# Kernel optimization log

Hardware: AMD Instinct MI355X
Metric: run time of the kernel (lower is better)

The kernel has to match this reference:

```python
import jax, jax.numpy as jnp
import numpy as np

IN_CH, OUT_CH = 64, 32
V1, V2 = 40962, 163842  # icosahedral levels; V2 = 4*V1 - 6
B = 4
EPS = 1e-5
SLOPE = 0.2  # LeakyReLU negative slope


def setup_inputs() -> dict:
    key = jax.random.key(0)
    ks = jax.random.split(key, 8)
    return {
        "x1": jax.random.normal(ks[0], (B, IN_CH, V1), jnp.float32),
        "x2": jax.random.normal(ks[1], (B, OUT_CH, V2), jnp.float32),
        "neigh_orders": jax.random.randint(ks[2], (7 * V2,), 0, V2, jnp.int32),
        "upconv_top_index": jax.random.randint(ks[3], (V1,), 0, V1 * 7, jnp.int32),
        "upconv_down_index": jax.random.randint(ks[4], (2 * (V2 - V1),), 0, V1 * 7, jnp.int32),
        "W_up": jax.random.normal(ks[5], (7 * OUT_CH, IN_CH), jnp.float32) * 0.05,
        "b_up": jnp.zeros((7 * OUT_CH,), jnp.float32),
        "W1": jax.random.normal(ks[6], (OUT_CH, 7 * 2 * OUT_CH), jnp.float32) * 0.05,
        "b1": jnp.zeros((OUT_CH,), jnp.float32),
        "g1": jnp.ones((OUT_CH,), jnp.float32),
        "be1": jnp.zeros((OUT_CH,), jnp.float32),
        "W2": jax.random.normal(ks[7], (OUT_CH, 7 * OUT_CH), jnp.float32) * 0.05,
        "b2": jnp.zeros((OUT_CH,), jnp.float32),
        "g2": jnp.ones((OUT_CH,), jnp.float32),
        "be2": jnp.zeros((OUT_CH,), jnp.float32),
    }


def _bn_lrelu(x, g, b):
    # BatchNorm1d with track_running_stats=False: always uses current (per-sample) batch stats,
    # biased variance, over the vertex axis. Then LeakyReLU(0.2).
    mu = x.mean(axis=0)
    var = x.var(axis=0)  # biased (ddof=0), matches torch BN normalization
    y = (x - mu) * jax.lax.rsqrt(var + EPS) * g + b
    return jnp.where(y >= 0, y, SLOPE * y)


def _one_sample(x1b, x2b, neigh, top, down,
                W_up, b_up, W1, b1, g1, be1, W2, b2, g2, be2):
    # upconv: Linear(in_ch -> 7*out_ch), scatter to the finer mesh via index gathers
    raw = x1b.T @ W_up.T + b_up                      # (V1, 7*OUT_CH)
    flat = raw.reshape(V1 * 7, OUT_CH)
    y_top = flat[top]                                # (V1, OUT_CH)
    y_down = flat[down].reshape(-1, OUT_CH, 2).mean(axis=-1)  # (V2-V1, OUT_CH), torch view semantics
    y1 = jnp.concatenate([y_top, y_down], axis=0)    # (V2, OUT_CH)
    y = jnp.concatenate([y1, x2b.T], axis=1)         # (V2, 2*OUT_CH) skip-concat
    # one-ring conv 1: gather 7 neighbors, flatten, GEMM
    m = y[neigh].reshape(V2, 7 * 2 * OUT_CH)
    h = _bn_lrelu(m @ W1.T + b1, g1, be1)            # (V2, OUT_CH)
    # one-ring conv 2
    m2 = h[neigh].reshape(V2, 7 * OUT_CH)
    h2 = _bn_lrelu(m2 @ W2.T + b2, g2, be2)          # (V2, OUT_CH)
    return h2.T                                      # (OUT_CH, V2)


def reference(x1, x2, neigh_orders, upconv_top_index, upconv_down_index,
              W_up, b_up, W1, b1, g1, be1, W2, b2, g2, be2):
    f = lambda a, b: _one_sample(a, b, neigh_orders, upconv_top_index, upconv_down_index,
                                 W_up, b_up, W1, b1, g1, be1, W2, b2, g2, be2)
    return jax.vmap(f)(x1, x2)  # (B, OUT_CH, V2)
```

## Files before the change

### kernel.cpp

```cpp
#include <hip/hip_runtime.h>

#define V1n 40962
#define V2n 163842
#define Bn  4

typedef _Float16 h8   __attribute__((ext_vector_type(8)));
typedef float    f32x4 __attribute__((ext_vector_type(4)));

__device__ __forceinline__ float h2f(_Float16 h) { return (float)h; }

__global__ __launch_bounds__(256) void k_pack_up(const float* __restrict__ Wup,
                                                 _Float16* __restrict__ WupP) {
  int i = blockIdx.x * 256 + threadIdx.x;
  if (i >= 14336) return;
  int e = i & 7, col = (i >> 3) & 15, g = i >> 7;
  int nt = g % 14, kq = g / 14;
  int j = nt * 16 + col;
  int k = (kq >> 2) * 32 + (kq & 3) * 8 + e;
  WupP[i] = (_Float16)Wup[j * 64 + k];
}

__global__ __launch_bounds__(256, 4) void k_upconv(const float* __restrict__ x1,
    const float* __restrict__ bup, const _Float16* __restrict__ WupP,
    _Float16* __restrict__ rawq) {
  int b = blockIdx.y;
  int lane = threadIdx.x & 63, wv = threadIdx.x >> 6;
  int col = lane & 15, quad = lane >> 4;
  int v0 = blockIdx.x * 64 + wv * 16;
  int v = v0 + col;
  int vc = min(v, V1n - 1);
  const float* xb = x1 + (size_t)b * 64 * V1n + vc;
  float t0[8], t1v[8];
#pragma unroll
  for (int e = 0; e < 8; ++e) t0[e] = xb[(size_t)(quad * 8 + e) * V1n];
#pragma unroll
  for (int e = 0; e < 8; ++e) t1v[e] = xb[(size_t)(32 + quad * 8 + e) * V1n];
  h8 a0, a1;
#pragma unroll
  for (int e = 0; e < 8; ++e) { a0[e] = (_Float16)t0[e]; a1[e] = (_Float16)t1v[e]; }

  f32x4 acc[14];
#pragma unroll
  for (int nt = 0; nt < 14; ++nt) {
    float bv = bup[nt * 16 + col];
    acc[nt] = (f32x4){bv, bv, bv, bv};
  }
  const _Float16* wp0 = WupP + (size_t)(quad * 14) * 128 + col * 8;
  const _Float16* wp1 = WupP + (size_t)((4 + quad) * 14) * 128 + col * 8;
#pragma unroll
  for (int nt = 0; nt < 14; ++nt) {
    h8 b0 = *(const h8*)(wp0 + nt * 128);
    acc[nt] = __builtin_amdgcn_mfma_f32_16x16x32_f16(a0, b0, acc[nt], 0, 0, 0);
  }
#pragma unroll
  for (int nt = 0; nt < 14; ++nt) {
    h8 b1 = *(const h8*)(wp1 + nt * 128);
    acc[nt] = __builtin_amdgcn_mfma_f32_16x16x32_f16(a1, b1, acc[nt], 0, 0, 0);
  }
  __shared__ _Float16 tile[4][3584];
  _Float16* tw = tile[wv];
#pragma unroll
  for (int nt = 0; nt < 14; ++nt)
#pragma unroll
    for (int r = 0; r < 4; ++r)
      tw[(quad * 4 + r) * 224 + nt * 16 + col] = (_Float16)acc[nt][r];
  __syncthreads();
  _Float16* dst = rawq + ((size_t)b * V1n + v0) * 224;
  int rem = V1n - v0;
  if (rem >= 16) {
#pragma unroll
    for (int i = 0; i < 7; ++i)
      *(h8*)(dst + i * 512 + lane * 8) = *(const h8*)(tw + i * 512 + lane * 8);
  } else if (rem > 0) {
    for (int i = 0; i < 7; ++i) {
      int off = i * 512 + lane * 8;
      if (off / 224 < rem) *(h8*)(dst + off) = *(const h8*)(tw + off);
    }
  }
}

__global__ __launch_bounds__(256) void k_assemble(const float* __restrict__ x2,
    const int* __restrict__ top, const int* __restrict__ down,
    const _Float16* __restrict__ rawq, _Float16* __restrict__ y) {
  int b = blockIdx.y;
  int v = blockIdx.x * 256 + threadIdx.x;
  if (v >= V2n) return;
  const _Float16* rb = rawq + (size_t)b * V1n * 224;
  h8 r0, r1, r2, r3;
  if (v < V1n) {
    int f = top[v];
    const _Float16* src = rb + (size_t)(f / 7) * 224 + (f % 7) * 32;
    r0 = *(const h8*)src;        r1 = *(const h8*)(src + 8);
    r2 = *(const h8*)(src + 16); r3 = *(const h8*)(src + 24);
  } else {
    int k = v - V1n;
    int d0 = down[2 * k], d1 = down[2 * k + 1];
    const _Float16* se = rb + (size_t)(d0 / 7) * 224 + (d0 % 7) * 32;
    const _Float16* so = rb + (size_t)(d1 / 7) * 224 + (d1 % 7) * 32;
    h8 a0 = *(const h8*)se,        a1 = *(const h8*)(se + 8);
    h8 a2 = *(const h8*)(se + 16), a3 = *(const h8*)(se + 24);
    h8 c0 = *(const h8*)so,        c1 = *(const h8*)(so + 8);
    h8 c2 = *(const h8*)(so + 16), c3 = *(const h8*)(so + 24);
#pragma unroll
    for (int i = 0; i < 4; ++i) {
      r0[i]     = (_Float16)(0.5f * (h2f(a0[2 * i]) + h2f(a0[2 * i + 1])));
      r0[4 + i] = (_Float16)(0.5f * (h2f(a1[2 * i]) + h2f(a1[2 * i + 1])));
      r1[i]     = (_Float16)(0.5f * (h2f(a2[2 * i]) + h2f(a2[2 * i + 1])));
      r1[4 + i] = (_Float16)(0.5f * (h2f(a3[2 * i]) + h2f(a3[2 * i + 1])));
      r2[i]     = (_Float16)(0.5f * (h2f(c0[2 * i]) + h2f(c0[2 * i + 1])));
      r2[4 + i] = (_Float16)(0.5f * (h2f(c1[2 * i]) + h2f(c1[2 * i + 1])));
      r3[i]     = (_Float16)(0.5f * (h2f(c2[2 * i]) + h2f(c2[2 * i + 1])));
      r3[4 + i] = (_Float16)(0.5f * (h2f(c3[2 * i]) + h2f(c3[2 * i + 1])));
    }
  }
  _Float16* dst = y + ((size_t)b * V2n + v) * 64;
  *(h8*)(dst)      = r0; *(h8*)(dst + 8)  = r1;
  *(h8*)(dst + 16) = r2; *(h8*)(dst + 24) = r3;
  const float* xp = x2 + (size_t)b * 32 * V2n + v;
#pragma unroll
  for (int g2 = 0; g2 < 4; ++g2) {
    h8 px;
#pragma unroll
    for (int e = 0; e < 8; ++e) px[e] = (_Float16)xp[(size_t)(g2 * 8 + e) * V2n];
    *(h8*)(dst + 32 + g2 * 8) = px;
  }
}

__global__ __launch_bounds__(256) void k_pack(const float* __restrict__ W1,
    const float* __restrict__ W2, _Float16* __restrict__ W1p,
    _Float16* __restrict__ W2p) {
  int i = blockIdx.x * 256 + threadIdx.x;
  if (i < 14336) {
    int e = i & 7, o = (i >> 3) & 31, g = i >> 8;
    int k = (g >> 2) * 32 + (g & 3) * 8 + e;
    W1p[i] = (_Float16)W1[o * 448 + k];
  }
  int i2 = i - 14336;
  if (i2 >= 0 && i2 < 7168) {
    int e = i2 & 7, o = (i2 >> 3) & 31, g = i2 >> 8;
    int k = (g >> 2) * 32 + (g & 3) * 8 + e;
    W2p[i2] = (_Float16)W2[o * 224 + k];
  }
}

__global__ __launch_bounds__(256, 4) void k_conv1(const _Float16* __restrict__ y,
    const int* __restrict__ neigh, const _Float16* __restrict__ W1p,
    _Float16* __restrict__ t1, float* __restrict__ sumsR) {
  int b = blockIdx.y;
  int lane = threadIdx.x & 63, wv = threadIdx.x >> 6;
  int col = lane & 15, quad = lane >> 4;
  int v0 = blockIdx.x * 64 + wv * 16;
  int v = v0 + col;
  int vc = min(v, V2n - 1);
  const int* np = neigh + 7 * (size_t)vc;
  int idx[7];
#pragma unroll
  for (int j = 0; j < 7; ++j) idx[j] = np[j];
  const _Float16* yb = y + (size_t)b * V2n * 64 + quad * 8;
  h8 a[14];
#pragma unroll
  for (int j = 0; j < 7; ++j) {
    const _Float16* r = yb + (size_t)idx[j] * 64;
    a[2 * j]     = *(const h8*)r;
    a[2 * j + 1] = *(const h8*)(r + 32);
  }
  f32x4 acc0 = {0.f, 0.f, 0.f, 0.f}, acc1 = {0.f, 0.f, 0.f, 0.f};
  const _Float16* wp = W1p + quad * 256;
#pragma unroll
  for (int kt = 0; kt < 14; ++kt) {
    h8 b0 = *(const h8*)(wp + (size_t)kt * 1024 + col * 8);
    h8 b1 = *(const h8*)(wp + (size_t)kt * 1024 + (16 + col) * 8);
    acc0 = __builtin_amdgcn_mfma_f32_16x16x32_f16(a[kt], b0, acc0, 0, 0, 0);
    acc1 = __builtin_amdgcn_mfma_f32_16x16x32_f16(a[kt], b1, acc1, 0, 0, 0);
  }
  __shared__ _Float16 tile[4][16][32];
  __shared__ float red[4][4][16];
#pragma unroll
  for (int r = 0; r < 4; ++r) {
    tile[wv][quad * 4 + r][col]      = (_Float16)acc0[r];
    tile[wv][quad * 4 + r][16 + col] = (_Float16)acc1[r];
  }
  __syncthreads();
  int row = threadIdx.x >> 2, ch = threadIdx.x & 3;
  int vv = blockIdx.x * 64 + row;
  float s[8], q[8];
#pragma unroll
  for (int e = 0; e < 8; ++e) { s[e] = 0.f; q[e] = 0.f; }
  if (vv < V2n) {
    h8 val = *(const h8*)&tile[row >> 4][row & 15][ch * 8];
    *(h8*)(t1 + ((size_t)b * V2n + vv) * 32 + ch * 8) = val;
#pragma unroll
    for (int e = 0; e < 8; ++e) { float x = h2f(val[e]); s[e] = x; q[e] = x * x; }
  }
#pragma unroll
  for (int m = 4; m <= 32; m <<= 1) {
#pragma unroll
    for (int e = 0; e < 8; ++e) { s[e] += __shfl_xor(s[e], m); q[e] += __shfl_xor(q[e], m); }
  }
  if (lane < 4) {
#pragma unroll
    for (int e = 0; e < 8; ++e) { red[wv][lane][e] = s[e]; red[wv][lane][8 + e] = q[e]; }
  }
  __syncthreads();
  if (threadIdx.x < 64) {
    int chh = threadIdx.x >> 4, e = threadIdx.x & 15;
    float v4 = red[0][chh][e] + red[1][chh][e] + red[2][chh][e] + red[3][chh][e];
    int c = chh * 8 + (e & 7);
    int rep = blockIdx.x & 63;
    float* dst = sumsR + rep * 256 + ((e < 8) ? (b * 32 + c) : (128 + b * 32 + c));
    atomicAdd(dst, v4);
  }
}

__global__ void k_finalize(const float* __restrict__ sumsR, const float* __restrict__ g,
                           const float* __restrict__ be, float* __restrict__ sc,
                           float* __restrict__ sh) {
  int i = threadIdx.x;
  if (i >= 128) return;
  float s = 0.f, q = 0.f;
  for (int r = 0; r < 64; ++r) { s += sumsR[r * 256 + i]; q += sumsR[r * 256 + 128 + i]; }
  float inv = 1.0f / (float)V2n;
  float mu = s * inv;
  float var = fmaf(q, inv, -mu * mu);
  float rs = rsqrtf(var + 1e-5f);
  int o = i & 31;
  float scale = rs * g[o];
  sc[i] = scale;
  sh[i] = fmaf(-mu, scale, be[o]);
}

__global__ __launch_bounds__(256, 4) void k_conv2(const _Float16* __restrict__ t1,
    const int* __restrict__ neigh, const _Float16* __restrict__ W2p,
    const float* __restrict__ sc1, const float* __restrict__ sh1,
    float* __restrict__ out, float* __restrict__ sumsR) {
  int b = blockIdx.y;
  int lane = threadIdx.x & 63, wv = threadIdx.x >> 6;
  int col = lane & 15, quad = lane >> 4;
  int v0 = blockIdx.x * 64 + wv * 16;
  int v = v0 + col;
  int vc = min(v, V2n - 1);
  const int* np = neigh + 7 * (size_t)vc;
  int idx[7];
#pragma unroll
  for (int j = 0; j < 7; ++j) idx[j] = np[j];
  const _Float16* tb = t1 + (size_t)b * V2n * 32 + quad * 8;
  h8 raw[7];
#pragma unroll
  for (int j = 0; j < 7; ++j) raw[j] = *(const h8*)(tb + (size_t)idx[j] * 32);
  float sc[8], sh[8];
#pragma unroll
  for (int i = 0; i < 8; ++i) {
    sc[i] = sc1[b * 32 + quad * 8 + i];
    sh[i] = sh1[b * 32 + quad * 8 + i];
  }
  f32x4 acc0 = {0.f, 0.f, 0.f, 0.f}, acc1 = {0.f, 0.f, 0.f, 0.f};
  const _Float16* wp = W2p + quad * 256;
#pragma unroll
  for (int j = 0; j < 7; ++j) {
    h8 a;
#pragma unroll
    for (int e = 0; e < 8; ++e) {
      float f = fmaf(h2f(raw[j][e]), sc[e], sh[e]);
      f = fmaxf(f, 0.2f * f);
      a[e] = (_Float16)f;
    }
    h8 b0 = *(const h8*)(wp + (size_t)j * 1024 + col * 8);
    h8 b1 = *(const h8*)(wp + (size_t)j * 1024 + (16 + col) * 8);
    acc0 = __builtin_amdgcn_mfma_f32_16x16x32_f16(a, b0, acc0, 0, 0, 0);
    acc1 = __builtin_amdgcn_mfma_f32_16x16x32_f16(a, b1, acc1, 0, 0, 0);
  }
  float* ob = out + (size_t)b * 32 * V2n;
  int vrow = v0 + quad * 4;
  float s0 = 0.f, q0 = 0.f, s1 = 0.f, q1 = 0.f;
  if (blockIdx.x != gridDim.x - 1) {
    float* p0 = ob + (size_t)col * V2n + vrow;
    *(float2*)p0       = make_float2(acc0[0], acc0[1]);
    *(float2*)(p0 + 2) = make_float2(acc0[2], acc0[3]);
    float* p1 = ob + (size_t)(16 + col) * V2n + vrow;
    *(float2*)p1       = make_float2(acc1[0], acc1[1]);
    *(float2*)(p1 + 2) = make_float2(acc1[2], acc1[3]);
#pragma unroll
    for (int r = 0; r < 4; ++r) {
      s0 += acc0[r]; q0 += acc0[r] * acc0[r];
      s1 += acc1[r]; q1 += acc1[r] * acc1[r];
    }
  } else {
#pragma unroll
    for (int r = 0; r < 4; ++r) {
      if (vrow + r < V2n) {
        ob[(size_t)col * V2n + vrow + r]        = acc0[r];
        ob[(size_t)(16 + col) * V2n + vrow + r] = acc1[r];
        s0 += acc0[r]; q0 += acc0[r] * acc0[r];
        s1 += acc1[r]; q1 += acc1[r] * acc1[r];
      }
    }
  }
#pragma unroll
  for (int m = 16; m <= 32; m <<= 1) {
    s0 += __shfl_xor(s0, m); q0 += __shfl_xor(q0, m);
    s1 += __shfl_xor(s1, m); q1 += __shfl_xor(q1, m);
  }
  __shared__ float red2[4][16][4];
  if (lane < 16) {
    red2[wv][col][0] = s0; red2[wv][col][1] = q0;
    red2[wv][col][2] = s1; red2[wv][col][3] = q1;
  }
  __syncthreads();
  if (threadIdx.x < 64) {
    int cc = threadIdx.x & 15, which = threadIdx.x >> 4;
    float v4 = red2[0][cc][which] + red2[1][cc][which] +
               red2[2][cc][which] + red2[3][cc][which];
    int c = (which & 2) ? cc + 16 : cc;
    int rep = blockIdx.x & 63;
    float* dst = sumsR + rep * 256 + ((which & 1) ? (128 + b * 32 + c) : (b * 32 + c));
    atomicAdd(dst, v4);
  }
}

__global__ __launch_bounds__(256) void k_bnorm(float* __restrict__ out,
    const float* __restrict__ sc, const float* __restrict__ sh) {
  int row = blockIdx.y, qrt = blockIdx.x;
  float scale = sc[row], shift = sh[row];
  float* p = out + (size_t)row * V2n;
  int i0 = qrt * 20480;
  int iend = (qrt == 3) ? 81921 : i0 + 20480;
  for (int i = i0 + (int)threadIdx.x; i < iend; i += 256) {
    float2 x = *(float2*)(p + 2 * (size_t)i);
    float a = fmaf(x.x, scale, shift); a = fmaxf(a, 0.2f * a);
    float b = fmaf(x.y, scale, shift); b = fmaxf(b, 0.2f * b);
    *(float2*)(p + 2 * (size_t)i) = make_float2(a, b);
  }
}

extern "C" void kernel_launch(void* const* d_in, const int* in_sizes, int n_in,
                              void* d_out, int out_size, void* d_ws, size_t ws_size,
                              hipStream_t stream) {
  const float* x1   = (const float*)d_in[0];
  const float* x2   = (const float*)d_in[1];
  const int*   neigh= (const int*)d_in[2];
  const int*   top  = (const int*)d_in[3];
  const int*   down = (const int*)d_in[4];
  const float* Wup  = (const float*)d_in[5];
  const float* bup  = (const float*)d_in[6];
  const float* W1   = (const float*)d_in[7];
  const float* g1   = (const float*)d_in[9];
  const float* be1  = (const float*)d_in[10];
  const float* W2   = (const float*)d_in[11];
  const float* g2   = (const float*)d_in[13];
  const float* be2  = (const float*)d_in[14];
  float* out = (float*)d_out;

  char* ws = (char*)d_ws;
  _Float16* rawq = (_Float16*)ws;
  _Float16* y    = (_Float16*)(ws + 73403904);
  _Float16* t1   = (_Float16*)(ws + 157291008);
  float* stats   = (float*)(ws + 199234560);
  float* sc1 = stats;        float* sh1 = stats + 128;
  float* sc2 = stats + 256;  float* sh2 = stats + 384;
  _Float16* WupP = t1;
  _Float16* W1p  = rawq;
  _Float16* W2p  = rawq + 14336;
  float* sumsR1 = (float*)(ws + (1 << 20));
  float* sumsR2 = (float*)(ws + (1 << 20) + 65536);

  k_pack_up  <<<56, 256, 0, stream>>>(Wup, WupP);
  k_upconv   <<<dim3(641, Bn),  256, 0, stream>>>(x1, bup, WupP, rawq);
  k_assemble <<<dim3(641, Bn),  256, 0, stream>>>(x2, top, down, rawq, y);
  k_pack     <<<84, 256, 0, stream>>>(W1, W2, W1p, W2p);
  hipMemsetAsync(sumsR1, 0, 131072, stream);
  k_conv1    <<<dim3(2561, Bn), 256, 0, stream>>>(y, neigh, W1p, t1, sumsR1);
  k_finalize <<<1, 128, 0, stream>>>(sumsR1, g1, be1, sc1, sh1);
  k_conv2    <<<dim3(2561, Bn), 256, 0, stream>>>(t1, neigh, W2p, sc1, sh1, out, sumsR2);
  k_finalize <<<1, 128, 0, stream>>>(sumsR2, g2, be2, sc2, sh2);
  k_bnorm    <<<dim3(4, 128),   256, 0, stream>>>(out, sc2, sh2);
}
```

Baseline: 503.9 us.

## Interleave batch in intermediate layouts and fuse batches in conv2 with fp16 staging

```diff
diff --git a/kernel.cpp b/kernel.cpp
--- a/kernel.cpp
+++ b/kernel.cpp
@@ -5,6 +5,7 @@
 #define Bn  4
 
 typedef _Float16 h8   __attribute__((ext_vector_type(8)));
+typedef _Float16 h2   __attribute__((ext_vector_type(2)));
 typedef float    f32x4 __attribute__((ext_vector_type(4)));
 
 __device__ __forceinline__ float h2f(_Float16 h) { return (float)h; }
@@ -23,58 +24,56 @@
 __global__ __launch_bounds__(256, 4) void k_upconv(const float* __restrict__ x1,
     const float* __restrict__ bup, const _Float16* __restrict__ WupP,
     _Float16* __restrict__ rawq) {
-  int b = blockIdx.y;
   int lane = threadIdx.x & 63, wv = threadIdx.x >> 6;
   int col = lane & 15, quad = lane >> 4;
   int v0 = blockIdx.x * 64 + wv * 16;
   int v = v0 + col;
   int vc = min(v, V1n - 1);
-  const float* xb = x1 + (size_t)b * 64 * V1n + vc;
-  float t0[8], t1v[8];
-#pragma unroll
-  for (int e = 0; e < 8; ++e) t0[e] = xb[(size_t)(quad * 8 + e) * V1n];
-#pragma unroll
-  for (int e = 0; e < 8; ++e) t1v[e] = xb[(size_t)(32 + quad * 8 + e) * V1n];
-  h8 a0, a1;
-#pragma unroll
-  for (int e = 0; e < 8; ++e) { a0[e] = (_Float16)t0[e]; a1[e] = (_Float16)t1v[e]; }
-
-  f32x4 acc[14];
-#pragma unroll
-  for (int nt = 0; nt < 14; ++nt) {
-    float bv = bup[nt * 16 + col];
-    acc[nt] = (f32x4){bv, bv, bv, bv};
-  }
+  __shared__ _Float16 tile[4][16 * 232];
+  _Float16* tw = tile[wv];
+  float bias[14];
+#pragma unroll
+  for (int nt = 0; nt < 14; ++nt) bias[nt] = bup[nt * 16 + col];
   const _Float16* wp0 = WupP + (size_t)(quad * 14) * 128 + col * 8;
   const _Float16* wp1 = WupP + (size_t)((4 + quad) * 14) * 128 + col * 8;
-#pragma unroll
-  for (int nt = 0; nt < 14; ++nt) {
-    h8 b0 = *(const h8*)(wp0 + nt * 128);
-    acc[nt] = __builtin_amdgcn_mfma_f32_16x16x32_f16(a0, b0, acc[nt], 0, 0, 0);
-  }
-#pragma unroll
-  for (int nt = 0; nt < 14; ++nt) {
-    h8 b1 = *(const h8*)(wp1 + nt * 128);
-    acc[nt] = __builtin_amdgcn_mfma_f32_16x16x32_f16(a1, b1, acc[nt], 0, 0, 0);
-  }
-  __shared__ _Float16 tile[4][3584];
-  _Float16* tw = tile[wv];
-#pragma unroll
-  for (int nt = 0; nt < 14; ++nt)
-#pragma unroll
-    for (int r = 0; r < 4; ++r)
-      tw[(quad * 4 + r) * 224 + nt * 16 + col] = (_Float16)acc[nt][r];
-  __syncthreads();
-  _Float16* dst = rawq + ((size_t)b * V1n + v0) * 224;
   int rem = V1n - v0;
-  if (rem >= 16) {
-#pragma unroll
-    for (int i = 0; i < 7; ++i)
-      *(h8*)(dst + i * 512 + lane * 8) = *(const h8*)(tw + i * 512 + lane * 8);
-  } else if (rem > 0) {
-    for (int i = 0; i < 7; ++i) {
-      int off = i * 512 + lane * 8;
-      if (off / 224 < rem) *(h8*)(dst + off) = *(const h8*)(tw + off);
+  int r = lane >> 2, part = lane & 3;
+  for (int b = 0; b < 4; ++b) {
+    const float* xb = x1 + ((size_t)b * 64) * V1n + vc;
+    h8 a0, a1;
+#pragma unroll
+    for (int e = 0; e < 8; ++e) a0[e] = (_Float16)xb[(size_t)(quad * 8 + e) * V1n];
+#pragma unroll
+    for (int e = 0; e < 8; ++e) a1[e] = (_Float16)xb[(size_t)(32 + quad * 8 + e) * V1n];
+    f32x4 acc[14];
+#pragma unroll
+    for (int nt = 0; nt < 14; ++nt) acc[nt] = (f32x4){bias[nt], bias[nt], bias[nt], bias[nt]};
+#pragma unroll
+    for (int nt = 0; nt < 14; ++nt) {
+      h8 bb = *(const h8*)(wp0 + nt * 128);
+      acc[nt] = __builtin_amdgcn_mfma_f32_16x16x32_f16(a0, bb, acc[nt], 0, 0, 0);
+    }
+#pragma unroll
+    for (int nt = 0; nt < 14; ++nt) {
+      h8 bb = *(const h8*)(wp1 + nt * 128);
+      acc[nt] = __builtin_amdgcn_mfma_f32_16x16x32_f16(a1, bb, acc[nt], 0, 0, 0);
+    }
+#pragma unroll
+    for (int nt = 0; nt < 14; ++nt)
+#pragma unroll
+      for (int rr = 0; rr < 4; ++rr)
+        tw[(quad * 4 + rr) * 232 + nt * 16 + col] = (_Float16)acc[nt][rr];
+    __syncthreads();
+    if (rem >= 16) {
+#pragma unroll
+      for (int g = 0; g < 7; ++g)
+        *(h8*)(rawq + (((size_t)(v0 + r) * 7 + g) * 4 + b) * 32 + part * 8) =
+            *(const h8*)(tw + r * 232 + g * 32 + part * 8);
+    } else if (rem > 0) {
+      for (int g = 0; g < 7; ++g)
+        if (r < rem)
+          *(h8*)(rawq + (((size_t)(v0 + r) * 7 + g) * 4 + b) * 32 + part * 8) =
+              *(const h8*)(tw + r * 232 + g * 32 + part * 8);
     }
   }
 }
@@ -82,21 +81,20 @@
 __global__ __launch_bounds__(256) void k_assemble(const float* __restrict__ x2,
     const int* __restrict__ top, const int* __restrict__ down,
     const _Float16* __restrict__ rawq, _Float16* __restrict__ y) {
-  int b = blockIdx.y;
-  int v = blockIdx.x * 256 + threadIdx.x;
+  int t = blockIdx.x * 256 + threadIdx.x;
+  int v = t >> 2, b = t & 3;
   if (v >= V2n) return;
-  const _Float16* rb = rawq + (size_t)b * V1n * 224;
   h8 r0, r1, r2, r3;
   if (v < V1n) {
     int f = top[v];
-    const _Float16* src = rb + (size_t)(f / 7) * 224 + (f % 7) * 32;
+    const _Float16* src = rawq + ((size_t)f * 4 + b) * 32;
     r0 = *(const h8*)src;        r1 = *(const h8*)(src + 8);
     r2 = *(const h8*)(src + 16); r3 = *(const h8*)(src + 24);
   } else {
     int k = v - V1n;
     int d0 = down[2 * k], d1 = down[2 * k + 1];
-    const _Float16* se = rb + (size_t)(d0 / 7) * 224 + (d0 % 7) * 32;
-    const _Float16* so = rb + (size_t)(d1 / 7) * 224 + (d1 % 7) * 32;
+    const _Float16* se = rawq + ((size_t)d0 * 4 + b) * 32;
+    const _Float16* so = rawq + ((size_t)d1 * 4 + b) * 32;
     h8 a0 = *(const h8*)se,        a1 = *(const h8*)(se + 8);
     h8 a2 = *(const h8*)(se + 16), a3 = *(const h8*)(se + 24);
     h8 c0 = *(const h8*)so,        c1 = *(const h8*)(so + 8);
@@ -188,7 +186,7 @@
   for (int e = 0; e < 8; ++e) { s[e] = 0.f; q[e] = 0.f; }
   if (vv < V2n) {
     h8 val = *(const h8*)&tile[row >> 4][row & 15][ch * 8];
-    *(h8*)(t1 + ((size_t)b * V2n + vv) * 32 + ch * 8) = val;
+    *(h8*)(t1 + ((size_t)vv * 4 + b) * 32 + ch * 8) = val;
 #pragma unroll
     for (int e = 0; e < 8; ++e) { float x = h2f(val[e]); s[e] = x; q[e] = x * x; }
   }
@@ -229,11 +227,10 @@
   sh[i] = fmaf(-mu, scale, be[o]);
 }
 
-__global__ __launch_bounds__(256, 4) void k_conv2(const _Float16* __restrict__ t1,
+__global__ __launch_bounds__(256, 3) void k_conv2(const _Float16* __restrict__ t1,
     const int* __restrict__ neigh, const _Float16* __restrict__ W2p,
     const float* __restrict__ sc1, const float* __restrict__ sh1,
-    float* __restrict__ out, float* __restrict__ sumsR) {
-  int b = blockIdx.y;
+    _Float16* __restrict__ t2, float* __restrict__ sumsR) {
   int lane = threadIdx.x & 63, wv = threadIdx.x >> 6;
   int col = lane & 15, quad = lane >> 4;
   int v0 = blockIdx.x * 64 + wv * 16;
@@ -243,92 +240,109 @@
   int idx[7];
 #pragma unroll
   for (int j = 0; j < 7; ++j) idx[j] = np[j];
-  const _Float16* tb = t1 + (size_t)b * V2n * 32 + quad * 8;
-  h8 raw[7];
-#pragma unroll
-  for (int j = 0; j < 7; ++j) raw[j] = *(const h8*)(tb + (size_t)idx[j] * 32);
-  float sc[8], sh[8];
-#pragma unroll
-  for (int i = 0; i < 8; ++i) {
-    sc[i] = sc1[b * 32 + quad * 8 + i];
-    sh[i] = sh1[b * 32 + quad * 8 + i];
-  }
-  f32x4 acc0 = {0.f, 0.f, 0.f, 0.f}, acc1 = {0.f, 0.f, 0.f, 0.f};
+  float sc[4][8], sh[4][8];
+#pragma unroll
+  for (int b = 0; b < 4; ++b)
+#pragma unroll
+    for (int i = 0; i < 8; ++i) {
+      sc[b][i] = sc1[b * 32 + quad * 8 + i];
+      sh[b][i] = sh1[b * 32 + quad * 8 + i];
+    }
+  f32x4 acc[4][2];
+#pragma unroll
+  for (int b = 0; b < 4; ++b) {
+    acc[b][0] = (f32x4){0.f, 0.f, 0.f, 0.f};
+    acc[b][1] = (f32x4){0.f, 0.f, 0.f, 0.f};
+  }
   const _Float16* wp = W2p + quad * 256;
 #pragma unroll
   for (int j = 0; j < 7; ++j) {
-    h8 a;
-#pragma unroll
-    for (int e = 0; e < 8; ++e) {
-      float f = fmaf(h2f(raw[j][e]), sc[e], sh[e]);
-      f = fmaxf(f, 0.2f * f);
-      a[e] = (_Float16)f;
-    }
-    h8 b0 = *(const h8*)(wp + (size_t)j * 1024 + col * 8);
-    h8 b1 = *(const h8*)(wp + (size_t)j * 1024 + (16 + col) * 8);
-    acc0 = __builtin_amdgcn_mfma_f32_16x16x32_f16(a, b0, acc0, 0, 0, 0);
-    acc1 = __builtin_amdgcn_mfma_f32_16x16x32_f16(a, b1, acc1, 0, 0, 0);
-  }
-  float* ob = out + (size_t)b * 32 * V2n;
+    const _Float16* r = t1 + (size_t)idx[j] * 128 + quad * 8;
+    h8 raws[4];
+#pragma unroll
+    for (int b = 0; b < 4; ++b) raws[b] = *(const h8*)(r + b * 32);
+    h8 w0 = *(const h8*)(wp + (size_t)j * 1024 + col * 8);
+    h8 w1 = *(const h8*)(wp + (size_t)j * 1024 + (16 + col) * 8);
+#pragma unroll
+    for (int b = 0; b < 4; ++b) {
+      h8 aa;
+#pragma unroll
+      for (int e = 0; e < 8; ++e) {
+        float f = fmaf(h2f(raws[b][e]), sc[b][e], sh[b][e]);
+        f = fmaxf(f, 0.2f * f);
+        aa[e] = (_Float16)f;
+      }
+      acc[b][0] = __builtin_amdgcn_mfma_f32_16x16x32_f16(aa, w0, acc[b][0], 0, 0, 0);
+      acc[b][1] = __builtin_amdgcn_mfma_f32_16x16x32_f16(aa, w1, acc[b][1], 0, 0, 0);
+    }
+  }
+  __shared__ float red2[4][16][4];
   int vrow = v0 + quad * 4;
-  float s0 = 0.f, q0 = 0.f, s1 = 0.f, q1 = 0.f;
-  if (blockIdx.x != gridDim.x - 1) {
-    float* p0 = ob + (size_t)col * V2n + vrow;
-    *(float2*)p0       = make_float2(acc0[0], acc0[1]);
-    *(float2*)(p0 + 2) = make_float2(acc0[2], acc0[3]);
-    float* p1 = ob + (size_t)(16 + col) * V2n + vrow;
-    *(float2*)p1       = make_float2(acc1[0], acc1[1]);
-    *(float2*)(p1 + 2) = make_float2(acc1[2], acc1[3]);
-#pragma unroll
-    for (int r = 0; r < 4; ++r) {
-      s0 += acc0[r]; q0 += acc0[r] * acc0[r];
-      s1 += acc1[r]; q1 += acc1[r] * acc1[r];
-    }
-  } else {
-#pragma unroll
-    for (int r = 0; r < 4; ++r) {
-      if (vrow + r < V2n) {
-        ob[(size_t)col * V2n + vrow + r]        = acc0[r];
-        ob[(size_t)(16 + col) * V2n + vrow + r] = acc1[r];
-        s0 += acc0[r]; q0 += acc0[r] * acc0[r];
-        s1 += acc1[r]; q1 += acc1[r] * acc1[r];
+  bool tailblk = (blockIdx.x == gridDim.x - 1);
+  int rep = blockIdx.x & 63;
+#pragma unroll
+  for (int b = 0; b < 4; ++b) {
+    if (b) __syncthreads();
+    float s0 = 0.f, q0 = 0.f, s1 = 0.f, q1 = 0.f;
+    _Float16* tb = t2 + (size_t)b * 32 * V2n;
+    if (!tailblk) {
+      _Float16* p0 = tb + (size_t)col * V2n + vrow;
+      _Float16* p1 = tb + (size_t)(16 + col) * V2n + vrow;
+      *(h2*)(p0)     = (h2){(_Float16)acc[b][0][0], (_Float16)acc[b][0][1]};
+      *(h2*)(p0 + 2) = (h2){(_Float16)acc[b][0][2], (_Float16)acc[b][0][3]};
+      *(h2*)(p1)     = (h2){(_Float16)acc[b][1][0], (_Float16)acc[b][1][1]};
+      *(h2*)(p1 + 2) = (h2){(_Float16)acc[b][1][2], (_Float16)acc[b][1][3]};
+#pragma unroll
+      for (int rr = 0; rr < 4; ++rr) {
+        s0 += acc[b][0][rr]; q0 += acc[b][0][rr] * acc[b][0][rr];
+        s1 += acc[b][1][rr]; q1 += acc[b][1][rr] * acc[b][1][rr];
       }
-    }
-  }
-#pragma unroll
-  for (int m = 16; m <= 32; m <<= 1) {
-    s0 += __shfl_xor(s0, m); q0 += __shfl_xor(q0, m);
-    s1 += __shfl_xor(s1, m); q1 += __shfl_xor(q1, m);
-  }
-  __shared__ float red2[4][16][4];
-  if (lane < 16) {
-    red2[wv][col][0] = s0; red2[wv][col][1] = q0;
-    red2[wv][col][2] = s1; red2[wv][col][3] = q1;
-  }
-  __syncthreads();
-  if (threadIdx.x < 64) {
-    int cc = threadIdx.x & 15, which = threadIdx.x >> 4;
-    float v4 = red2[0][cc][which] + red2[1][cc][which] +
-               red2[2][cc][which] + red2[3][cc][which];
-    int c = (which & 2) ? cc + 16 : cc;
-    int rep = blockIdx.x & 63;
-    float* dst = sumsR + rep * 256 + ((which & 1) ? (128 + b * 32 + c) : (b * 32 + c));
-    atomicAdd(dst, v4);
-  }
-}
-
-__global__ __launch_bounds__(256) void k_bnorm(float* __restrict__ out,
-    const float* __restrict__ sc, const float* __restrict__ sh) {
+    } else {
+#pragma unroll
+      for (int rr = 0; rr < 4; ++rr) {
+        if (vrow + rr < V2n) {
+          tb[(size_t)col * V2n + vrow + rr]        = (_Float16)acc[b][0][rr];
+          tb[(size_t)(16 + col) * V2n + vrow + rr] = (_Float16)acc[b][1][rr];
+          s0 += acc[b][0][rr]; q0 += acc[b][0][rr] * acc[b][0][rr];
+          s1 += acc[b][1][rr]; q1 += acc[b][1][rr] * acc[b][1][rr];
+        }
+      }
+    }
+#pragma unroll
+    for (int m = 16; m <= 32; m <<= 1) {
+      s0 += __shfl_xor(s0, m); q0 += __shfl_xor(q0, m);
+      s1 += __shfl_xor(s1, m); q1 += __shfl_xor(q1, m);
+    }
+    if (lane < 16) {
+      red2[wv][col][0] = s0; red2[wv][col][1] = q0;
+      red2[wv][col][2] = s1; red2[wv][col][3] = q1;
+    }
+    __syncthreads();
+    if (threadIdx.x < 64) {
+      int cc = threadIdx.x & 15, which = threadIdx.x >> 4;
+      float v4 = red2[0][cc][which] + red2[1][cc][which] +
+                 red2[2][cc][which] + red2[3][cc][which];
+      int c = (which & 2) ? cc + 16 : cc;
+      float* dstp = sumsR + rep * 256 + ((which & 1) ? (128 + b * 32 + c) : (b * 32 + c));
+      atomicAdd(dstp, v4);
+    }
+  }
+}
+
+__global__ __launch_bounds__(256) void k_bnorm(const _Float16* __restrict__ t2,
+    const float* __restrict__ sc, const float* __restrict__ sh,
+    float* __restrict__ out) {
   int row = blockIdx.y, qrt = blockIdx.x;
   float scale = sc[row], shift = sh[row];
-  float* p = out + (size_t)row * V2n;
+  const _Float16* p = t2 + (size_t)row * V2n;
+  float* o = out + (size_t)row * V2n;
   int i0 = qrt * 20480;
   int iend = (qrt == 3) ? 81921 : i0 + 20480;
   for (int i = i0 + (int)threadIdx.x; i < iend; i += 256) {
-    float2 x = *(float2*)(p + 2 * (size_t)i);
-    float a = fmaf(x.x, scale, shift); a = fmaxf(a, 0.2f * a);
-    float b = fmaf(x.y, scale, shift); b = fmaxf(b, 0.2f * b);
-    *(float2*)(p + 2 * (size_t)i) = make_float2(a, b);
+    h2 x = *(const h2*)(p + 2 * (size_t)i);
+    float a = fmaf((float)x[0], scale, shift); a = fmaxf(a, 0.2f * a);
+    float b = fmaf((float)x[1], scale, shift); b = fmaxf(b, 0.2f * b);
+    *(float2*)(o + 2 * (size_t)i) = make_float2(a, b);
   }
 }
 
@@ -362,15 +376,16 @@
   _Float16* W2p  = rawq + 14336;
   float* sumsR1 = (float*)(ws + (1 << 20));
   float* sumsR2 = (float*)(ws + (1 << 20) + 65536);
+  _Float16* t2  = (_Float16*)(ws + (2 << 20));
 
   k_pack_up  <<<56, 256, 0, stream>>>(Wup, WupP);
-  k_upconv   <<<dim3(641, Bn),  256, 0, stream>>>(x1, bup, WupP, rawq);
-  k_assemble <<<dim3(641, Bn),  256, 0, stream>>>(x2, top, down, rawq, y);
+  k_upconv   <<<641,  256, 0, stream>>>(x1, bup, WupP, rawq);
+  k_assemble <<<2561, 256, 0, stream>>>(x2, top, down, rawq, y);
   k_pack     <<<84, 256, 0, stream>>>(W1, W2, W1p, W2p);
   hipMemsetAsync(sumsR1, 0, 131072, stream);
   k_conv1    <<<dim3(2561, Bn), 256, 0, stream>>>(y, neigh, W1p, t1, sumsR1);
   k_finalize <<<1, 128, 0, stream>>>(sumsR1, g1, be1, sc1, sh1);
-  k_conv2    <<<dim3(2561, Bn), 256, 0, stream>>>(t1, neigh, W2p, sc1, sh1, out, sumsR2);
+  k_conv2    <<<2561, 256, 0, stream>>>(t1, neigh, W2p, sc1, sh1, t2, sumsR2);
   k_finalize <<<1, 128, 0, stream>>>(sumsR2, g2, be2, sc2, sh2);
-  k_bnorm    <<<dim3(4, 128),   256, 0, stream>>>(out, sc2, sh2);
-}
+  k_bnorm    <<<dim3(4, 128),   256, 0, stream>>>(t2, sc2, sh2, out);
+}
```

Result: slower. 589.6 us (+17.0%).
